# Kernel tuning notes

Hardware: AMD Instinct MI355X
Metric: run time of the kernel (lower is better)

Reference implementation:

```python
import jax, jax.numpy as jnp
import numpy as np

B, C, K, H, W = 8, 3, 4, 512, 512


def setup_inputs() -> dict:
    key = jax.random.key(0)
    k1, k2, k3, k4 = jax.random.split(key, 4)
    x = jax.random.normal(k1, (B, C, H, W), dtype=jnp.float32)
    U = jax.random.normal(k2, (B, C * K, H, W), dtype=jnp.float32)
    # V must exceed U^2 for meaningful variances (clamp still applied in reference)
    V = U ** 2 + jax.random.uniform(k3, (B, C * K, H, W), dtype=jnp.float32, minval=0.1, maxval=1.0)
    # N must be strictly positive (log, division by per-group sum)
    N = jax.random.uniform(k4, (B, C * K, H, W), dtype=jnp.float32, minval=0.1, maxval=1.0)
    eta = jnp.float32(0.01)
    return {"x": x, "U": U, "V": V, "N": N, "eta": eta}


def reference(x, U, V, N, eta):
    B, C, H, W = x.shape
    K = U.shape[1] // C
    # regroup channel*component axis -> (C, K) so per-channel group ops are vectorized
    Ug = U.reshape(B, C, K, H, W)
    Vg = V.reshape(B, C, K, H, W)
    Ng = N.reshape(B, C, K, H, W)

    S2 = jnp.maximum(Vg - Ug ** 2, 0.01)
    S = jnp.sqrt(S2)
    Xd = x[:, :, None, :, :] - Ug           # x broadcast over K (== X_cat - U)
    z = Xd / S

    nTotal = 1.0 / eta - 1.0
    Nn = nTotal * Ng / jnp.sum(Ng, axis=2, keepdims=True)  # renormalize counts per channel
    P = Nn / nTotal

    cdf = jax.scipy.stats.norm.cdf(jnp.abs(z))             # Normal(0,1).cdf(|z|)
    prob = jnp.sum(P * cdf, axis=2)                        # B x C x H x W

    log_prob = jnp.log(Nn) - 0.5 * z ** 2 - jnp.log(S)
    Gamma = jax.nn.softmax(log_prob, axis=2)               # softmax over K per channel

    N_out = Nn + Gamma
    Eta = Gamma / N_out
    U_out = Ug + Eta * Xd
    V_out = Vg + Eta * (x[:, :, None, :, :] ** 2 - Vg)

    CK = C * K
    return (U_out.reshape(B, CK, H, W),
            V_out.reshape(B, CK, H, W),
            N_out.reshape(B, CK, H, W),
            prob)
```

## Files before the change

kernel.cpp:

```cpp
#include <hip/hip_runtime.h>
#include <math.h>


typedef float f32x4 __attribute__((ext_vector_type(4)));

#define HALF_LOG2E 0.7213475204444817f
#define NI 8

__global__ __launch_bounds__(256) void gmm_kernel(
    const f32x4* __restrict__ x4,
    const f32x4* __restrict__ U4,
    const f32x4* __restrict__ V4,
    const f32x4* __restrict__ N4,
    const float* __restrict__ eta_p,
    float* __restrict__ out,
    int total,
    int ckhw4)
{
    const int HWQ = 65536;
    const float nTotal = 1.0f / eta_p[0] - 1.0f;

    f32x4* Uo = (f32x4*)out;
    f32x4* Vo = Uo + ckhw4;
    f32x4* No = Vo + ckhw4;
    f32x4* Po = No + ckhw4;

    const int t0 = blockIdx.x * (256 * NI) + threadIdx.x;

#pragma unroll 1
    for (int s = 0; s < NI; ++s) {
        const int t = t0 + s * 256;
        if (t >= total) break;

        const int bc = t >> 16;
        const int p4 = t & 65535;
        const int base = bc * 4 * HWQ + p4;

        const f32x4 xv = x4[t];
        f32x4 Uv[4], Vv[4], Nv[4];
#pragma unroll
        for (int k = 0; k < 4; ++k) {
            Uv[k] = U4[base + k * HWQ];
            Vv[k] = V4[base + k * HWQ];
            Nv[k] = N4[base + k * HWQ];
        }

        f32x4 Pw;

#pragma unroll
        for (int j = 0; j < 4; ++j) {
            const float xs = xv[j];

            float u[4], vv[4], nn[4];
            float nsum = 0.f;
#pragma unroll
            for (int k = 0; k < 4; ++k) {
                u[k]  = Uv[k][j];
                vv[k] = Vv[k][j];
                nn[k] = Nv[k][j];
                nsum += nn[k];
            }
            const float inv_nsum = __builtin_amdgcn_rcpf(nsum);

            float l2[4], Nn[4], Xd[4];
            float prob = 0.f;
            float m = -1e30f;
#pragma unroll
            for (int k = 0; k < 4; ++k) {
                const float uu   = u[k];
                const float s2   = fmaxf(vv[k] - uu * uu, 0.01f);
                const float invS = __builtin_amdgcn_rsqf(s2);
                const float xd   = xs - uu;
                const float z    = xd * invS;
                const float P    = nn[k] * inv_nsum;
                const float nnk  = nTotal * P;
                const float cdf  = 0.5f * (1.0f + erff(fabsf(z) * 0.70710678118654752440f));
                prob += P * cdf;
                const float l = __builtin_amdgcn_logf(nnk * invS) - HALF_LOG2E * z * z;
                l2[k] = l;
                m = fmaxf(m, l);
                Nn[k] = nnk;
                Xd[k] = xd;
            }

            float g[4], gs = 0.f;
#pragma unroll
            for (int k = 0; k < 4; ++k) { g[k] = __builtin_amdgcn_exp2f(l2[k] - m); gs += g[k]; }
            const float invgs = __builtin_amdgcn_rcpf(gs);
            const float x2 = xs * xs;

#pragma unroll
            for (int k = 0; k < 4; ++k) {
                const float Gamma = g[k] * invgs;
                const float Nout  = Nn[k] + Gamma;
                const float Eta   = Gamma * __builtin_amdgcn_rcpf(Nout);
                Uv[k][j] = u[k]  + Eta * Xd[k];
                Vv[k][j] = vv[k] + Eta * (x2 - vv[k]);
                Nv[k][j] = Nout;
            }
            Pw[j] = prob;
        }

#pragma unroll
        for (int k = 0; k < 4; ++k) {
            __builtin_nontemporal_store(Uv[k], &Uo[base + k * HWQ]);
            __builtin_nontemporal_store(Vv[k], &Vo[base + k * HWQ]);
            __builtin_nontemporal_store(Nv[k], &No[base + k * HWQ]);
        }
        __builtin_nontemporal_store(Pw, &Po[t]);
    }
}

extern "C" void kernel_launch(void* const* d_in, const int* in_sizes, int n_in,
                              void* d_out, int out_size, void* d_ws, size_t ws_size,
                              hipStream_t stream) {
    const f32x4* x  = (const f32x4*)d_in[0];
    const f32x4* U  = (const f32x4*)d_in[1];
    const f32x4* V  = (const f32x4*)d_in[2];
    const f32x4* N  = (const f32x4*)d_in[3];
    const float* eta = (const float*)d_in[4];
    float* out = (float*)d_out;

    const int total = in_sizes[0] / 4;
    const int ckhw4 = in_sizes[1] / 4;

    const int block = 256;
    const int items_per_block = block * NI;
    const int grid = (total + items_per_block - 1) / items_per_block;
    gmm_kernel<<<grid, block, 0, stream>>>(x, U, V, N, eta, out, total, ckhw4);
}
```

Baseline: 127.1 us.

## Double-buffer register loads across unrolled item loop to overlap memory and compute

After: 339.2 us. +166.8%, slower.

```diff
diff --git a/kernel.cpp b/kernel.cpp
--- a/kernel.cpp
+++ b/kernel.cpp
@@ -5,9 +5,107 @@
 typedef float f32x4 __attribute__((ext_vector_type(4)));
 
 #define HALF_LOG2E 0.7213475204444817f
-#define NI 8
+#define NI 4
+#define HWQ 65536
 
-__global__ __launch_bounds__(256) void gmm_kernel(
+struct Item {
+    f32x4 x;
+    f32x4 U[4], V[4], N[4];
+};
+
+__device__ __forceinline__ int item_base(int t) {
+    const int bc = t >> 16;
+    const int p4 = t & 65535;
+    return bc * 4 * HWQ + p4;
+}
+
+__device__ __forceinline__ void load_item(
+    Item& it, int t,
+    const f32x4* __restrict__ x4, const f32x4* __restrict__ U4,
+    const f32x4* __restrict__ V4, const f32x4* __restrict__ N4)
+{
+    const int base = item_base(t);
+    it.x = x4[t];
+#pragma unroll
+    for (int k = 0; k < 4; ++k) {
+        it.U[k] = U4[base + k * HWQ];
+        it.V[k] = V4[base + k * HWQ];
+        it.N[k] = N4[base + k * HWQ];
+    }
+}
+
+__device__ __forceinline__ void compute_store_item(
+    Item& it, int t, float nTotal,
+    f32x4* __restrict__ Uo, f32x4* __restrict__ Vo,
+    f32x4* __restrict__ No, f32x4* __restrict__ Po)
+{
+    const int base = item_base(t);
+    f32x4 Pw;
+
+#pragma unroll
+    for (int j = 0; j < 4; ++j) {
+        const float xs = it.x[j];
+
+        float u[4], vv[4], nn[4];
+        float nsum = 0.f;
+#pragma unroll
+        for (int k = 0; k < 4; ++k) {
+            u[k]  = it.U[k][j];
+            vv[k] = it.V[k][j];
+            nn[k] = it.N[k][j];
+            nsum += nn[k];
+        }
+        const float inv_nsum = __builtin_amdgcn_rcpf(nsum);
+
+        float l2[4], Nn[4], Xd[4];
+        float prob = 0.f;
+        float m = -1e30f;
+#pragma unroll
+        for (int k = 0; k < 4; ++k) {
+            const float uu   = u[k];
+            const float s2   = fmaxf(vv[k] - uu * uu, 0.01f);
+            const float invS = __builtin_amdgcn_rsqf(s2);
+            const float xd   = xs - uu;
+            const float z    = xd * invS;
+            const float P    = nn[k] * inv_nsum;
+            const float nnk  = nTotal * P;
+            const float cdf  = 0.5f * (1.0f + erff(fabsf(z) * 0.70710678118654752440f));
+            prob += P * cdf;
+            const float l = __builtin_amdgcn_logf(nnk * invS) - HALF_LOG2E * z * z;
+            l2[k] = l;
+            m = fmaxf(m, l);
+            Nn[k] = nnk;
+            Xd[k] = xd;
+        }
+
+        float g[4], gs = 0.f;
+#pragma unroll
+        for (int k = 0; k < 4; ++k) { g[k] = __builtin_amdgcn_exp2f(l2[k] - m); gs += g[k]; }
+        const float invgs = __builtin_amdgcn_rcpf(gs);
+        const float x2 = xs * xs;
+
+#pragma unroll
+        for (int k = 0; k < 4; ++k) {
+            const float Gamma = g[k] * invgs;
+            const float Nout  = Nn[k] + Gamma;
+            const float Eta   = Gamma * __builtin_amdgcn_rcpf(Nout);
+            it.U[k][j] = u[k]  + Eta * Xd[k];
+            it.V[k][j] = vv[k] + Eta * (x2 - vv[k]);
+            it.N[k][j] = Nout;
+        }
+        Pw[j] = prob;
+    }
+
+#pragma unroll
+    for (int k = 0; k < 4; ++k) {
+        __builtin_nontemporal_store(it.U[k], &Uo[base + k * HWQ]);
+        __builtin_nontemporal_store(it.V[k], &Vo[base + k * HWQ]);
+        __builtin_nontemporal_store(it.N[k], &No[base + k * HWQ]);
+    }
+    __builtin_nontemporal_store(Pw, &Po[t]);
+}
+
+__global__ __launch_bounds__(256, 4) void gmm_kernel(
     const f32x4* __restrict__ x4,
     const f32x4* __restrict__ U4,
     const f32x4* __restrict__ V4,
@@ -17,7 +115,6 @@
     int total,
     int ckhw4)
 {
-    const int HWQ = 65536;
     const float nTotal = 1.0f / eta_p[0] - 1.0f;
 
     f32x4* Uo = (f32x4*)out;
@@ -27,87 +124,14 @@
 
     const int t0 = blockIdx.x * (256 * NI) + threadIdx.x;
 
-#pragma unroll 1
-    for (int s = 0; s < NI; ++s) {
-        const int t = t0 + s * 256;
-        if (t >= total) break;
-
-        const int bc = t >> 16;
-        const int p4 = t & 65535;
-        const int base = bc * 4 * HWQ + p4;
-
-        const f32x4 xv = x4[t];
-        f32x4 Uv[4], Vv[4], Nv[4];
-#pragma unroll
-        for (int k = 0; k < 4; ++k) {
-            Uv[k] = U4[base + k * HWQ];
-            Vv[k] = V4[base + k * HWQ];
-            Nv[k] = N4[base + k * HWQ];
-        }
-
-        f32x4 Pw;
+    Item buf[2];
+    load_item(buf[0], t0, x4, U4, V4, N4);
 
 #pragma unroll
-        for (int j = 0; j < 4; ++j) {
-            const float xs = xv[j];
-
-            float u[4], vv[4], nn[4];
-            float nsum = 0.f;
-#pragma unroll
-            for (int k = 0; k < 4; ++k) {
-                u[k]  = Uv[k][j];
-                vv[k] = Vv[k][j];
-                nn[k] = Nv[k][j];
-                nsum += nn[k];
-            }
-            const float inv_nsum = __builtin_amdgcn_rcpf(nsum);
-
-            float l2[4], Nn[4], Xd[4];
-            float prob = 0.f;
-            float m = -1e30f;
-#pragma unroll
-            for (int k = 0; k < 4; ++k) {
-                const float uu   = u[k];
-                const float s2   = fmaxf(vv[k] - uu * uu, 0.01f);
-                const float invS = __builtin_amdgcn_rsqf(s2);
-                const float xd   = xs - uu;
-                const float z    = xd * invS;
-                const float P    = nn[k] * inv_nsum;
-                const float nnk  = nTotal * P;
-                const float cdf  = 0.5f * (1.0f + erff(fabsf(z) * 0.70710678118654752440f));
-                prob += P * cdf;
-                const float l = __builtin_amdgcn_logf(nnk * invS) - HALF_LOG2E * z * z;
-                l2[k] = l;
-                m = fmaxf(m, l);
-                Nn[k] = nnk;
-                Xd[k] = xd;
-            }
-
-            float g[4], gs = 0.f;
-#pragma unroll
-            for (int k = 0; k < 4; ++k) { g[k] = __builtin_amdgcn_exp2f(l2[k] - m); gs += g[k]; }
-            const float invgs = __builtin_amdgcn_rcpf(gs);
-            const float x2 = xs * xs;
-
-#pragma unroll
-            for (int k = 0; k < 4; ++k) {
-                const float Gamma = g[k] * invgs;
-                const float Nout  = Nn[k] + Gamma;
-                const float Eta   = Gamma * __builtin_amdgcn_rcpf(Nout);
-                Uv[k][j] = u[k]  + Eta * Xd[k];
-                Vv[k][j] = vv[k] + Eta * (x2 - vv[k]);
-                Nv[k][j] = Nout;
-            }
-            Pw[j] = prob;
-        }
-
-#pragma unroll
-        for (int k = 0; k < 4; ++k) {
-            __builtin_nontemporal_store(Uv[k], &Uo[base + k * HWQ]);
-            __builtin_nontemporal_store(Vv[k], &Vo[base + k * HWQ]);
-            __builtin_nontemporal_store(Nv[k], &No[base + k * HWQ]);
-        }
-        __builtin_nontemporal_store(Pw, &Po[t]);
+    for (int s = 0; s < NI; ++s) {
+        if (s + 1 < NI)
+            load_item(buf[(s + 1) & 1], t0 + (s + 1) * 256, x4, U4, V4, N4);
+        compute_store_item(buf[s & 1], t0 + s * 256, nTotal, Uo, Vo, No, Po);
     }
 }
 
```
